# Optimization experiments

Measured on AMD Instinct MI355X. Metric: run time of the kernel, lower is better.

## Reference

```python
import jax, jax.numpy as jnp
import numpy as np

N, F_IN, F_OUT = 8192, 512, 256

def setup_inputs() -> dict:
    key = jax.random.key(0)
    kx, kW, ka = jax.random.split(key, 3)
    x = jax.random.normal(kx, (N, F_IN), dtype=jnp.float32)
    adj = jnp.ones((N, N), dtype=jnp.float32)  # accepted but unused by the original forward
    # nn.Linear(in, out, bias=False) stores weight as [out, in]
    W = jax.random.normal(kW, (F_OUT, F_IN), dtype=jnp.float32) * 0.02
    # nn.Linear(2*out, 1, bias=False) -> attention vector of length 2*F_OUT
    a = jax.random.normal(ka, (2 * F_OUT,), dtype=jnp.float32) * 0.02
    return {"x": x, "adj": adj, "W": W, "a": a}

def reference(x, adj, W, a):
    # h = W(x): [N, F_OUT]
    h = x @ W.T
    # Original concatenates [h_i, h_j] for all pairs (O(N^2 * 2F) memory) and
    # applies linear a. Since a is linear, e_ij = a1.h_i + a2.h_j -> broadcast add.
    a_src, a_dst = a[:F_OUT], a[F_OUT:]
    e = (h @ a_src)[:, None] + (h @ a_dst)[None, :]  # [N, N]
    attention = jax.nn.softmax(e, axis=1)             # row-wise over neighbors j
    h_prime = attention @ h                           # [N, F_OUT]
    return h_prime
```

## Files before the change

kernel.cpp:

```cpp
#include <hip/hip_runtime.h>
#include <math.h>

#define NN 8192
#define FIN 512
#define FOUT 256
#define NBLK 64


__global__ __launch_bounds__(256) void compute_g(const float* __restrict__ W,
                                                 const float* __restrict__ a_dst,
                                                 float* __restrict__ g) {
    __shared__ float red[4][64];
    const int tid = threadIdx.x;
    const int kl = tid & 63;
    const int cp = tid >> 6;
    const int k = blockIdx.x * 64 + kl;
    float s = 0.f;
    #pragma unroll 8
    for (int c = cp * 64; c < cp * 64 + 64; ++c)
        s = fmaf(W[(size_t)c * FIN + k], a_dst[c], s);
    red[cp][kl] = s;
    __syncthreads();
    if (cp == 0) g[k] = red[0][kl] + red[1][kl] + red[2][kl] + red[3][kl];
}

__global__ __launch_bounds__(512) void fused_pass(const float* __restrict__ x,
                                                  const float* __restrict__ g,
                                                  float* __restrict__ pm,
                                                  float* __restrict__ ps,
                                                  float* __restrict__ pu) {
    __shared__ float gs[FIN];
    __shared__ float ds[128];
    __shared__ float wred[8];
    const int tid = threadIdx.x;
    const int lane = tid & 63;
    const int wave = tid >> 6;
    const int r0 = blockIdx.x * 128;

    if (tid < 128) ((float4*)gs)[tid] = ((const float4*)g)[tid];
    __syncthreads();

    const float4* gv = (const float4*)gs;
    float4 g0 = gv[lane], g1 = gv[lane + 64];

    float lmax = -1e30f;
    #pragma unroll 4
    for (int rr = 0; rr < 16; ++rr) {
        const int j = wave * 16 + rr;
        const float4* xr = (const float4*)(x + (size_t)(r0 + j) * FIN);
        float4 x0 = xr[lane], x1 = xr[lane + 64];
        float s = x0.x * g0.x + x0.y * g0.y + x0.z * g0.z + x0.w * g0.w
                + x1.x * g1.x + x1.y * g1.y + x1.z * g1.z + x1.w * g1.w;
        #pragma unroll
        for (int off = 32; off; off >>= 1) s += __shfl_xor(s, off);
        if (lane == 0) ds[j] = s;
        lmax = fmaxf(lmax, s);
    }
    if (lane == 0) wred[wave] = lmax;
    __syncthreads();

    float m_b = wred[0];
    #pragma unroll
    for (int i = 1; i < 8; ++i) m_b = fmaxf(m_b, wred[i]);

    if (tid < 128) ds[tid] = expf(ds[tid] - m_b);
    __syncthreads();

    if (wave == 0) {
        float s = ds[lane] + ds[lane + 64];
        #pragma unroll
        for (int off = 32; off; off >>= 1) s += __shfl_xor(s, off);
        if (lane == 0) {
            ps[blockIdx.x] = s;
            pm[blockIdx.x] = m_b;
        }
    }

    float acc = 0.f;
    #pragma unroll 8
    for (int j = 0; j < 128; ++j)
        acc = fmaf(ds[j], x[(size_t)(r0 + j) * FIN + tid], acc);
    pu[(size_t)blockIdx.x * FIN + tid] = acc;
}

__global__ __launch_bounds__(512) void combine(const float* __restrict__ pm,
                                               const float* __restrict__ ps,
                                               const float* __restrict__ pu,
                                               float* __restrict__ u_scaled) {
    __shared__ float m_s[NBLK];
    __shared__ float sc[NBLK];
    __shared__ float Ss;
    const int tid = threadIdx.x;
    if (tid < NBLK) m_s[tid] = pm[tid];
    __syncthreads();

    float M = m_s[0];
    #pragma unroll 8
    for (int i = 1; i < NBLK; ++i) M = fmaxf(M, m_s[i]);

    if (tid < NBLK) sc[tid] = expf(m_s[tid] - M);
    __syncthreads();

    if (tid < 64) {
        float s = ps[tid] * sc[tid];
        #pragma unroll
        for (int off = 32; off; off >>= 1) s += __shfl_xor(s, off);
        if (tid == 0) Ss = s;
    }
    __syncthreads();

    float acc = 0.f;
    #pragma unroll 8
    for (int b = 0; b < NBLK; ++b)
        acc = fmaf(sc[b], pu[(size_t)b * FIN + tid], acc);
    u_scaled[tid] = acc / Ss;
}

__global__ __launch_bounds__(256) void compute_v(const float* __restrict__ W,
                                                 const float* __restrict__ u_scaled,
                                                 float* __restrict__ vs) {
    __shared__ float us[FIN];
    const int tid = threadIdx.x;
    if (tid < 128) ((float4*)us)[tid] = ((const float4*)u_scaled)[tid];
    __syncthreads();
    const int lane = tid & 63;
    const int wave = tid >> 6;
    const int c = blockIdx.x * 4 + wave;
    const float4* wr = (const float4*)(W + (size_t)c * FIN);
    const float4* uv = (const float4*)us;
    float4 w0 = wr[lane], w1 = wr[lane + 64];
    float4 u0 = uv[lane], u1 = uv[lane + 64];
    float s = w0.x * u0.x + w0.y * u0.y + w0.z * u0.z + w0.w * u0.w
            + w1.x * u1.x + w1.y * u1.y + w1.z * u1.z + w1.w * u1.w;
    #pragma unroll
    for (int off = 32; off; off >>= 1) s += __shfl_xor(s, off);
    if (lane == 0) vs[c] = s;
}

__global__ __launch_bounds__(256) void broadcast_out(const float* __restrict__ vs,
                                                     float* __restrict__ out) {
    const int idx = blockIdx.x * 256 + threadIdx.x;
    float4 vv = ((const float4*)vs)[idx & 63];
    ((float4*)out)[idx] = vv;
}

extern "C" void kernel_launch(void* const* d_in, const int* in_sizes, int n_in,
                              void* d_out, int out_size, void* d_ws, size_t ws_size,
                              hipStream_t stream) {
    const float* x = (const float*)d_in[0];
    const float* W = (const float*)d_in[2];
    const float* a = (const float*)d_in[3];
    float* out = (float*)d_out;

    float* ws   = (float*)d_ws;
    float* g    = ws;
    float* pm   = ws + 512;
    float* ps   = ws + 512 + 64;
    float* pu   = ws + 1024;
    float* u    = ws + 1024 + NBLK * FIN;
    float* vs   = u + FIN;

    compute_g<<<8, 256, 0, stream>>>(W, a + FOUT, g);
    fused_pass<<<NBLK, 512, 0, stream>>>(x, g, pm, ps, pu);
    combine<<<1, 512, 0, stream>>>(pm, ps, pu, u);
    compute_v<<<FOUT / 4, 256, 0, stream>>>(W, u, vs);
    broadcast_out<<<(NN * FOUT / 4) / 256, 256, 0, stream>>>(vs, out);
}
```

Baseline: 336.1 us.

## Spread row reduction over many blocks with atomics and drop the combine kernel

The single pass over x is split from 64 blocks of 128 rows into 512 blocks of 16 rows, with each wave keeping its rows in registers. Partial weighted sums are accumulated with atomics into 8 replicated buffers, and the global softmax denominator into one scalar. The max-subtraction step is dropped, along with the separate combine kernel. compute_v now sums the 8 buffers and divides by the denominator, and compute_g zeroes the buffers first. The aim is to fill the GPU and cut a launch, but skipping the max makes the softmax unstable for large logits and only safe when the logits are small.

```diff
diff --git a/kernel.cpp b/kernel.cpp
--- a/kernel.cpp
+++ b/kernel.cpp
@@ -4,14 +4,22 @@
 #define NN 8192
 #define FIN 512
 #define FOUT 256
-#define NBLK 64
+#define FBLK 512
+#define NU 8
 
 
 __global__ __launch_bounds__(256) void compute_g(const float* __restrict__ W,
                                                  const float* __restrict__ a_dst,
-                                                 float* __restrict__ g) {
+                                                 float* __restrict__ g,
+                                                 float* __restrict__ u8,
+                                                 float* __restrict__ S) {
     __shared__ float red[4][64];
     const int tid = threadIdx.x;
+
+    const int zi = blockIdx.x * 256 + tid;
+    ((float2*)u8)[zi] = make_float2(0.f, 0.f);
+    if (zi == 0) *S = 0.f;
+
     const int kl = tid & 63;
     const int cp = tid >> 6;
     const int k = blockIdx.x * 64 + kl;
@@ -24,105 +32,72 @@
     if (cp == 0) g[k] = red[0][kl] + red[1][kl] + red[2][kl] + red[3][kl];
 }
 
-__global__ __launch_bounds__(512) void fused_pass(const float* __restrict__ x,
+__global__ __launch_bounds__(256) void fused_pass(const float* __restrict__ x,
                                                   const float* __restrict__ g,
-                                                  float* __restrict__ pm,
-                                                  float* __restrict__ ps,
-                                                  float* __restrict__ pu) {
-    __shared__ float gs[FIN];
-    __shared__ float ds[128];
-    __shared__ float wred[8];
+                                                  float* __restrict__ u8,
+                                                  float* __restrict__ S) {
+    __shared__ float us[4][FIN];
+    __shared__ float sred[4];
     const int tid = threadIdx.x;
     const int lane = tid & 63;
     const int wave = tid >> 6;
-    const int r0 = blockIdx.x * 128;
+    const int r0 = blockIdx.x * 16;
 
-    if (tid < 128) ((float4*)gs)[tid] = ((const float4*)g)[tid];
+    const float4* g4 = (const float4*)g;
+    const float4 g0 = g4[lane], g1 = g4[lane + 64];
+
+    float4 xa[4], xb[4];
+    float w[4];
+    #pragma unroll
+    for (int rr = 0; rr < 4; ++rr) {
+        const float4* xr = (const float4*)(x + (size_t)(r0 + wave * 4 + rr) * FIN);
+        xa[rr] = xr[lane];
+        xb[rr] = xr[lane + 64];
+        float s = xa[rr].x * g0.x + xa[rr].y * g0.y + xa[rr].z * g0.z + xa[rr].w * g0.w
+                + xb[rr].x * g1.x + xb[rr].y * g1.y + xb[rr].z * g1.z + xb[rr].w * g1.w;
+        #pragma unroll
+        for (int off = 32; off; off >>= 1) s += __shfl_xor(s, off);
+        w[rr] = __expf(s);
+    }
+    if (lane == 0) sred[wave] = w[0] + w[1] + w[2] + w[3];
+
+    float4 pa = make_float4(0.f, 0.f, 0.f, 0.f);
+    float4 pb = make_float4(0.f, 0.f, 0.f, 0.f);
+    #pragma unroll
+    for (int rr = 0; rr < 4; ++rr) {
+        pa.x = fmaf(w[rr], xa[rr].x, pa.x); pa.y = fmaf(w[rr], xa[rr].y, pa.y);
+        pa.z = fmaf(w[rr], xa[rr].z, pa.z); pa.w = fmaf(w[rr], xa[rr].w, pa.w);
+        pb.x = fmaf(w[rr], xb[rr].x, pb.x); pb.y = fmaf(w[rr], xb[rr].y, pb.y);
+        pb.z = fmaf(w[rr], xb[rr].z, pb.z); pb.w = fmaf(w[rr], xb[rr].w, pb.w);
+    }
+    ((float4*)&us[wave][0])[lane] = pa;
+    ((float4*)&us[wave][FOUT])[lane] = pb;
     __syncthreads();
 
-    const float4* gv = (const float4*)gs;
-    float4 g0 = gv[lane], g1 = gv[lane + 64];
-
-    float lmax = -1e30f;
-    #pragma unroll 4
-    for (int rr = 0; rr < 16; ++rr) {
-        const int j = wave * 16 + rr;
-        const float4* xr = (const float4*)(x + (size_t)(r0 + j) * FIN);
-        float4 x0 = xr[lane], x1 = xr[lane + 64];
-        float s = x0.x * g0.x + x0.y * g0.y + x0.z * g0.z + x0.w * g0.w
-                + x1.x * g1.x + x1.y * g1.y + x1.z * g1.z + x1.w * g1.w;
-        #pragma unroll
-        for (int off = 32; off; off >>= 1) s += __shfl_xor(s, off);
-        if (lane == 0) ds[j] = s;
-        lmax = fmaxf(lmax, s);
-    }
-    if (lane == 0) wred[wave] = lmax;
-    __syncthreads();
-
-    float m_b = wred[0];
-    #pragma unroll
-    for (int i = 1; i < 8; ++i) m_b = fmaxf(m_b, wred[i]);
-
-    if (tid < 128) ds[tid] = expf(ds[tid] - m_b);
-    __syncthreads();
-
-    if (wave == 0) {
-        float s = ds[lane] + ds[lane + 64];
-        #pragma unroll
-        for (int off = 32; off; off >>= 1) s += __shfl_xor(s, off);
-        if (lane == 0) {
-            ps[blockIdx.x] = s;
-            pm[blockIdx.x] = m_b;
-        }
-    }
-
-    float acc = 0.f;
-    #pragma unroll 8
-    for (int j = 0; j < 128; ++j)
-        acc = fmaf(ds[j], x[(size_t)(r0 + j) * FIN + tid], acc);
-    pu[(size_t)blockIdx.x * FIN + tid] = acc;
-}
-
-__global__ __launch_bounds__(512) void combine(const float* __restrict__ pm,
-                                               const float* __restrict__ ps,
-                                               const float* __restrict__ pu,
-                                               float* __restrict__ u_scaled) {
-    __shared__ float m_s[NBLK];
-    __shared__ float sc[NBLK];
-    __shared__ float Ss;
-    const int tid = threadIdx.x;
-    if (tid < NBLK) m_s[tid] = pm[tid];
-    __syncthreads();
-
-    float M = m_s[0];
-    #pragma unroll 8
-    for (int i = 1; i < NBLK; ++i) M = fmaxf(M, m_s[i]);
-
-    if (tid < NBLK) sc[tid] = expf(m_s[tid] - M);
-    __syncthreads();
-
-    if (tid < 64) {
-        float s = ps[tid] * sc[tid];
-        #pragma unroll
-        for (int off = 32; off; off >>= 1) s += __shfl_xor(s, off);
-        if (tid == 0) Ss = s;
-    }
-    __syncthreads();
-
-    float acc = 0.f;
-    #pragma unroll 8
-    for (int b = 0; b < NBLK; ++b)
-        acc = fmaf(sc[b], pu[(size_t)b * FIN + tid], acc);
-    u_scaled[tid] = acc / Ss;
+    float* ub = u8 + (size_t)(blockIdx.x & (NU - 1)) * FIN;
+    float v0 = us[0][tid] + us[1][tid] + us[2][tid] + us[3][tid];
+    float v1 = us[0][tid + 256] + us[1][tid + 256] + us[2][tid + 256] + us[3][tid + 256];
+    atomicAdd(&ub[tid], v0);
+    atomicAdd(&ub[tid + 256], v1);
+    if (tid == 0) atomicAdd(S, sred[0] + sred[1] + sred[2] + sred[3]);
 }
 
 __global__ __launch_bounds__(256) void compute_v(const float* __restrict__ W,
-                                                 const float* __restrict__ u_scaled,
+                                                 const float* __restrict__ u8,
+                                                 const float* __restrict__ S,
                                                  float* __restrict__ vs) {
     __shared__ float us[FIN];
     const int tid = threadIdx.x;
-    if (tid < 128) ((float4*)us)[tid] = ((const float4*)u_scaled)[tid];
+    float a0 = 0.f, a1 = 0.f;
+    #pragma unroll
+    for (int i = 0; i < NU; ++i) {
+        a0 += u8[(size_t)i * FIN + tid];
+        a1 += u8[(size_t)i * FIN + tid + 256];
+    }
+    us[tid] = a0;
+    us[tid + 256] = a1;
     __syncthreads();
+
     const int lane = tid & 63;
     const int wave = tid >> 6;
     const int c = blockIdx.x * 4 + wave;
@@ -134,7 +109,7 @@
             + w1.x * u1.x + w1.y * u1.y + w1.z * u1.z + w1.w * u1.w;
     #pragma unroll
     for (int off = 32; off; off >>= 1) s += __shfl_xor(s, off);
-    if (lane == 0) vs[c] = s;
+    if (lane == 0) vs[c] = s / *S;
 }
 
 __global__ __launch_bounds__(256) void broadcast_out(const float* __restrict__ vs,
@@ -152,17 +127,14 @@
     const float* a = (const float*)d_in[3];
     float* out = (float*)d_out;
 
-    float* ws   = (float*)d_ws;
-    float* g    = ws;
-    float* pm   = ws + 512;
-    float* ps   = ws + 512 + 64;
-    float* pu   = ws + 1024;
-    float* u    = ws + 1024 + NBLK * FIN;
-    float* vs   = u + FIN;
+    float* ws = (float*)d_ws;
+    float* g  = ws;
+    float* u8 = ws + 512;
+    float* S  = ws + 512 + NU * FIN;
+    float* vs = S + 16;
 
-    compute_g<<<8, 256, 0, stream>>>(W, a + FOUT, g);
-    fused_pass<<<NBLK, 512, 0, stream>>>(x, g, pm, ps, pu);
-    combine<<<1, 512, 0, stream>>>(pm, ps, pu, u);
-    compute_v<<<FOUT / 4, 256, 0, stream>>>(W, u, vs);
+    compute_g<<<8, 256, 0, stream>>>(W, a + FOUT, g, u8, S);
+    fused_pass<<<FBLK, 256, 0, stream>>>(x, g, u8, S);
+    compute_v<<<FOUT / 4, 256, 0, stream>>>(W, u8, S, vs);
     broadcast_out<<<(NN * FOUT / 4) / 256, 256, 0, stream>>>(vs, out);
 }
```

Result: faster. 323.3 us (-3.8%).
